# Kernel tuning notes

Measured on AMD Instinct MI355X. Metric: run time of the kernel, lower is better.

Reference implementation:

```python
import jax, jax.numpy as jnp
import numpy as np

B, S, HID = 2, 2048, 1024
H, D = 16, HID // 16  # heads, head_dim
ROPE_BASE = 10000.0


def setup_inputs() -> dict:
    key = jax.random.key(0)
    k1, k2, k3, k4 = jax.random.split(key, 4)
    scale = 1.0 / np.sqrt(HID)
    return {
        "hidden_states": jax.random.normal(k1, (B, S, HID), dtype=jnp.float32),
        "attention_mask": jnp.zeros((B, 1, 1, S), dtype=jnp.float32),
        "Wq": jax.random.normal(k2, (HID, HID), dtype=jnp.float32) * scale,
        "Wk": jax.random.normal(k3, (HID, HID), dtype=jnp.float32) * scale,
        "Wv": jax.random.normal(k4, (HID, HID), dtype=jnp.float32) * scale,
    }


def _rope_cos_sin(seq_len, dim, dtype):
    inv_freq = 1.0 / (ROPE_BASE ** (jnp.arange(0, dim, 2, dtype=jnp.float32) / dim))
    freqs = jnp.arange(seq_len, dtype=jnp.float32)[:, None] * inv_freq[None, :]  # (S, D/2)
    emb = jnp.concatenate([freqs, freqs], axis=-1)  # (S, D)
    return jnp.cos(emb).astype(dtype), jnp.sin(emb).astype(dtype)


def _rotate_half(x):
    x1, x2 = jnp.split(x, 2, axis=-1)
    return jnp.concatenate([-x2, x1], axis=-1)


def reference(hidden_states, attention_mask, Wq, Wk, Wv):
    b, s, _ = hidden_states.shape
    # QKV projections (no bias), split into heads: (b, H, s, D)
    def proj(W):
        return jnp.einsum('bse,de->bsd', hidden_states, W).reshape(b, s, H, D).transpose(0, 2, 1, 3)
    q, k, v = proj(Wq), proj(Wk), proj(Wv)
    # Rotary embedding on q, k over sequence positions
    cos, sin = _rope_cos_sin(s, D, hidden_states.dtype)  # (s, D)
    cos = cos[None, None]  # (1,1,s,D)
    sin = sin[None, None]
    q = q * cos + _rotate_half(q) * sin
    k = k * cos + _rotate_half(k) * sin
    # Scaled dot-product attention with additive mask
    scores = jnp.einsum('bhqd,bhkd->bhqk', q, k) / jnp.sqrt(jnp.asarray(D, hidden_states.dtype))
    scores = scores + attention_mask
    probs = jax.nn.softmax(scores, axis=-1)  # dropout p=0 (eval) -> identity
    ctx = jnp.einsum('bhqk,bhkd->bhqd', probs, v)
    return ctx.transpose(0, 2, 1, 3).reshape(b, s, H * D)
```

## Files before the change

### kernel.cpp

```cpp
#include <hip/hip_runtime.h>
#include <stdint.h>

typedef unsigned short u16;
typedef short bf16x8 __attribute__((ext_vector_type(8)));
typedef float f32x4 __attribute__((ext_vector_type(4)));

#define S_ 2048
#define HID_ 1024
#define H_ 16
#define D_ 64

#define LOG2E 1.4426950408889634f
#define SCALE_LOG2 0.18033688011112042f
#define MAXC_LOG2 11.541560327111707f

__device__ __forceinline__ u16 f2bf(float f) {
  uint32_t x = __builtin_bit_cast(uint32_t, f);
  uint32_t r = (x + 0x7fffu + ((x >> 16) & 1u)) >> 16;
  return (u16)r;
}
__device__ __forceinline__ uint32_t packbf2(float a, float b) {
  return (uint32_t)f2bf(a) | ((uint32_t)f2bf(b) << 16);
}
__device__ __forceinline__ uint32_t permpack(float a, float b) {
  return __builtin_amdgcn_perm(__builtin_bit_cast(uint32_t, b),
                               __builtin_bit_cast(uint32_t, a), 0x07060302u);
}

__device__ __forceinline__ void gl2lds16(const void* g, void* l) {
  __builtin_amdgcn_global_load_lds(
      (const __attribute__((address_space(1))) unsigned int*)g,
      (__attribute__((address_space(3))) unsigned int*)l, 16, 0, 0);
}

#define NX_ (1 << 20)
#define NW_ (1 << 18)
#define NROPE_ 65536
__global__ void prep_kernel(const float* __restrict__ X, const float* __restrict__ Wq,
                            const float* __restrict__ Wk, const float* __restrict__ Wv,
                            const float* __restrict__ mask, u16* __restrict__ Xb,
                            u16* __restrict__ Wqb, u16* __restrict__ Wkb,
                            u16* __restrict__ Wvb, float* __restrict__ cos_t,
                            float* __restrict__ sin_t, float* __restrict__ mask2) {
  int i = blockIdx.x * 256 + threadIdx.x;
  if (i < NX_ + 3 * NW_) {
    const float* src;
    u16* dst;
    int off;
    if (i < NX_) {
      src = X; dst = Xb; off = i;
    } else if (i < NX_ + NW_) {
      src = Wq; dst = Wqb; off = i - NX_;
    } else if (i < NX_ + 2 * NW_) {
      src = Wk; dst = Wkb; off = i - NX_ - NW_;
    } else {
      src = Wv; dst = Wvb; off = i - NX_ - 2 * NW_;
    }
    float4 v = ((const float4*)src)[off];
    uint2 packed;
    packed.x = packbf2(v.x, v.y);
    packed.y = packbf2(v.z, v.w);
    ((uint2*)dst)[off] = packed;
  } else if (i < NX_ + 3 * NW_ + NROPE_) {
    int t = i - (NX_ + 3 * NW_);
    int s = t >> 5, j = t & 31;
    float invf = powf(10000.0f, -(float)j * (1.0f / 32.0f));
    float ang = (float)s * invf;
    cos_t[t] = cosf(ang);
    sin_t[t] = sinf(ang);
  } else {
    int t = i - (NX_ + 3 * NW_ + NROPE_);
    mask2[t] = fmaf(mask[t], LOG2E, -MAXC_LOG2);
  }
}

__global__ __launch_bounds__(256) void qkv_gemm_kernel(
    const u16* __restrict__ X, const u16* __restrict__ Wq, const u16* __restrict__ Wk,
    const u16* __restrict__ Wv, const float* __restrict__ cos_t,
    const float* __restrict__ sin_t, u16* __restrict__ Q, u16* __restrict__ K,
    u16* __restrict__ Vt) {
  __shared__ char smem[65536];
  int tid = threadIdx.x;
  int lane = tid & 63, wave = tid >> 6;
  int wm = wave >> 1, wn = wave & 1;
  int quad = lane >> 4, l16 = lane & 15;
  int which = blockIdx.x >> 3;
  int nbase = (blockIdx.x & 7) * 128;
  int mbase = blockIdx.y * 128;
  const u16* W = (which == 0) ? Wq : (which == 1) ? Wk : Wv;

#pragma unroll
  for (int it = 0; it < 4; ++it) {
    int i = it * 256 + tid;
    int r = i >> 3, gs = i & 7, gsrc = gs ^ (r & 7);
    gl2lds16(X + (size_t)(mbase + r) * HID_ + gsrc * 8, smem + i * 16);
    gl2lds16(W + (size_t)(nbase + r) * HID_ + gsrc * 8, smem + 32768 + i * 16);
  }

  f32x4 acc[4][4] = {};

  for (int kk = 0; kk < 16; ++kk) {
    char* As = smem + (kk & 1) * 16384;
    char* Bs = smem + 32768 + (kk & 1) * 16384;
    __syncthreads();

    if (kk < 15) {
      int k0n = (kk + 1) * 64;
      char* An = smem + ((kk + 1) & 1) * 16384;
      char* Bn = smem + 32768 + ((kk + 1) & 1) * 16384;
#pragma unroll
      for (int it = 0; it < 4; ++it) {
        int i = it * 256 + tid;
        int r = i >> 3, gs = i & 7, gsrc = gs ^ (r & 7);
        gl2lds16(X + (size_t)(mbase + r) * HID_ + k0n + gsrc * 8, An + i * 16);
        gl2lds16(W + (size_t)(nbase + r) * HID_ + k0n + gsrc * 8, Bn + i * 16);
      }
    }

#pragma unroll
    for (int kh = 0; kh < 2; ++kh) {
      bf16x8 afrag[4], bfrag[4];
#pragma unroll
      for (int i4 = 0; i4 < 4; ++i4) {
        int r = wm * 64 + i4 * 16 + l16;
        int L = r * 8 + ((kh * 4 + quad) ^ (r & 7));
        afrag[i4] = *(const bf16x8*)(As + L * 16);
      }
#pragma unroll
      for (int j4 = 0; j4 < 4; ++j4) {
        int r = wn * 64 + j4 * 16 + l16;
        int L = r * 8 + ((kh * 4 + quad) ^ (r & 7));
        bfrag[j4] = *(const bf16x8*)(Bs + L * 16);
      }
      if (which == 2) {
#pragma unroll
        for (int i4 = 0; i4 < 4; ++i4)
#pragma unroll
          for (int j4 = 0; j4 < 4; ++j4)
            acc[i4][j4] = __builtin_amdgcn_mfma_f32_16x16x32_bf16(afrag[i4], bfrag[j4],
                                                                  acc[i4][j4], 0, 0, 0);
      } else {
#pragma unroll
        for (int i4 = 0; i4 < 4; ++i4)
#pragma unroll
          for (int j4 = 0; j4 < 4; ++j4)
            acc[i4][j4] = __builtin_amdgcn_mfma_f32_16x16x32_bf16(bfrag[j4], afrag[i4],
                                                                  acc[i4][j4], 0, 0, 0);
      }
    }
  }

  if (which == 2) {
#pragma unroll
    for (int i4 = 0; i4 < 4; ++i4)
#pragma unroll
      for (int j4 = 0; j4 < 4; ++j4) {
        int m = mbase + wm * 64 + i4 * 16 + quad * 4;
        int n = nbase + wn * 64 + j4 * 16 + l16;
        int b = m >> 11, s0 = m & 2047;
        int h = n >> 6, d = n & 63;
        uint2 pk;
        pk.x = packbf2(acc[i4][j4][0], acc[i4][j4][1]);
        pk.y = packbf2(acc[i4][j4][2], acc[i4][j4][3]);
        *(uint2*)(Vt + (((size_t)(b * H_ + h)) * D_ + d) * S_ + s0) = pk;
      }
  } else {
    u16* dst = (which == 0) ? Q : K;
#pragma unroll
    for (int i4 = 0; i4 < 4; ++i4)
#pragma unroll
      for (int j4 = 0; j4 < 2; ++j4) {
        int m = mbase + wm * 64 + i4 * 16 + l16;
        int n1 = nbase + wn * 64 + j4 * 16 + quad * 4;
        int b = m >> 11, s = m & 2047;
        int h = n1 >> 6, d1 = n1 & 63;
        float4 c4 = *(const float4*)(cos_t + s * 32 + d1);
        float4 s4 = *(const float4*)(sin_t + s * 32 + d1);
        float y1[4], y2[4];
#pragma unroll
        for (int r = 0; r < 4; ++r) {
          float cr = ((const float*)&c4)[r], sr = ((const float*)&s4)[r];
          float x1 = acc[i4][j4][r], x2 = acc[i4][j4 + 2][r];
          y1[r] = x1 * cr - x2 * sr;
          y2[r] = x2 * cr + x1 * sr;
        }
        size_t base = ((size_t)(b * H_ + h) * S_ + s) * D_;
        uint2 p1, p2;
        p1.x = packbf2(y1[0], y1[1]);
        p1.y = packbf2(y1[2], y1[3]);
        p2.x = packbf2(y2[0], y2[1]);
        p2.y = packbf2(y2[2], y2[3]);
        *(uint2*)(dst + base + d1) = p1;
        *(uint2*)(dst + base + d1 + 32) = p2;
      }
  }
}

__device__ __forceinline__ void pv_step(const bf16x8 (*pp)[2], const char* Vp, int quad,
                                        int l16, const bf16x8& ones, f32x4 (*o)[4],
                                        f32x4* lacc) {
  lacc[0] = __builtin_amdgcn_mfma_f32_16x16x32_bf16(pp[0][0], ones, lacc[0], 0, 0, 0);
  lacc[0] = __builtin_amdgcn_mfma_f32_16x16x32_bf16(pp[0][1], ones, lacc[0], 0, 0, 0);
  lacc[1] = __builtin_amdgcn_mfma_f32_16x16x32_bf16(pp[1][0], ones, lacc[1], 0, 0, 0);
  lacc[1] = __builtin_amdgcn_mfma_f32_16x16x32_bf16(pp[1][1], ones, lacc[1], 0, 0, 0);
#pragma unroll
  for (int jd = 0; jd < 4; ++jd) {
    int r = jd * 16 + l16;
#pragma unroll
    for (int kh = 0; kh < 2; ++kh) {
      int L = r * 8 + ((kh * 4 + quad) ^ (r & 7));
      bf16x8 vf = *(const bf16x8*)(Vp + L * 16);
      o[0][jd] = __builtin_amdgcn_mfma_f32_16x16x32_bf16(pp[0][kh], vf, o[0][jd], 0, 0, 0);
      o[1][jd] = __builtin_amdgcn_mfma_f32_16x16x32_bf16(pp[1][kh], vf, o[1][jd], 0, 0, 0);
    }
  }
}

__device__ __forceinline__ void qk_step(const char* Ks, const bf16x8 (*qfrag)[2], int quad,
                                        int l16, f32x4 (*s)[4]) {
#pragma unroll
  for (int jt = 0; jt < 4; ++jt) {
    int r = jt * 16 + l16;
#pragma unroll
    for (int kh = 0; kh < 2; ++kh) {
      int L = r * 8 + ((kh * 4 + quad) ^ (r & 7));
      bf16x8 kf = *(const bf16x8*)(Ks + L * 16);
      s[0][jt] = __builtin_amdgcn_mfma_f32_16x16x32_bf16(kf, qfrag[0][kh], s[0][jt], 0, 0, 0);
      s[1][jt] = __builtin_amdgcn_mfma_f32_16x16x32_bf16(kf, qfrag[1][kh], s[1][jt], 0, 0, 0);
    }
  }
}

__device__ __forceinline__ void softmax_pack(const f32x4 (*s)[4], const float4* mv,
                                             bf16x8 (*pp)[2]) {
#pragma unroll
  for (int qb = 0; qb < 2; ++qb) {
    uint32_t a[4][2];
#pragma unroll
    for (int jt = 0; jt < 4; ++jt) {
      float pf[4];
#pragma unroll
      for (int r = 0; r < 4; ++r) {
        float mvr = ((const float*)&mv[jt])[r];
        pf[r] = __builtin_amdgcn_exp2f(fmaf(s[qb][jt][r], SCALE_LOG2, mvr));
      }
      a[jt][0] = permpack(pf[0], pf[1]);
      a[jt][1] = permpack(pf[2], pf[3]);
    }
#pragma unroll
    for (int kh = 0; kh < 2; ++kh) {
      uint32_t tt[4];
#pragma unroll
      for (int i = 0; i < 2; ++i) {
        auto r1 = __builtin_amdgcn_permlane32_swap(a[2 * kh][i], a[2 * kh + 1][i],
                                                   false, false);
        auto r2 = __builtin_amdgcn_permlane16_swap(r1[0], r1[1], false, false);
        tt[i] = r2[0];
        tt[2 + i] = r2[1];
      }
      union { uint32_t u[4]; bf16x8 v; } cv;
      cv.u[0] = tt[0]; cv.u[1] = tt[1]; cv.u[2] = tt[2]; cv.u[3] = tt[3];
      pp[qb][kh] = cv.v;
    }
  }
}

__device__ __forceinline__ void stage_kv(const u16* Kbase, const u16* Vbase, char* Kn,
                                         int nb, int tid) {
#pragma unroll
  for (int half = 0; half < 2; ++half) {
    int i = half * 256 + tid;
    int r = i >> 3, gs = i & 7, gsrc = gs ^ (r & 7);
    gl2lds16(Kbase + (size_t)(nb + r) * D_ + gsrc * 8, Kn + i * 16);
    gl2lds16(Vbase + (size_t)r * S_ + nb + gsrc * 8, Kn + 8192 + i * 16);
  }
}

__global__ __launch_bounds__(256, 2) void flash_kernel(
    const u16* __restrict__ Q, const u16* __restrict__ K, const u16* __restrict__ Vt,
    const float* __restrict__ mask2, float* __restrict__ out) {
  __shared__ char smem[49152];
  int tid = threadIdx.x, wave = tid >> 6;
  int lane = tid & 63;
  int quad = lane >> 4, l16 = lane & 15;
  int bh = blockIdx.y, b = bh >> 4, h = bh & 15;
  int qbase = blockIdx.x * 128;
  int qw = qbase + wave * 32;
  const float* m2row = mask2 + b * S_;
  const u16* Kbase = K + (size_t)bh * S_ * D_;
  const u16* Vbase = Vt + (size_t)bh * D_ * S_;

  bf16x8 qfrag[2][2];
#pragma unroll
  for (int qb = 0; qb < 2; ++qb) {
    const u16* qp = Q + ((size_t)bh * S_ + qw + qb * 16 + l16) * D_ + quad * 8;
    qfrag[qb][0] = *(const bf16x8*)qp;
    qfrag[qb][1] = *(const bf16x8*)(qp + 32);
  }
  bf16x8 ones;
#pragma unroll
  for (int j = 0; j < 8; ++j) ones[j] = (short)0x3f80;

  f32x4 o[2][4] = {};
  f32x4 lacc[2] = {};
  bf16x8 pp[2][2];

  stage_kv(Kbase, Vbase, smem, 0, tid);
  float4 mv[4];
#pragma unroll
  for (int jt = 0; jt < 4; ++jt) mv[jt] = *(const float4*)(m2row + jt * 16 + quad * 4);

  {
    __syncthreads();
    stage_kv(Kbase, Vbase, smem + 16384, 64, tid);
    f32x4 s[2][4] = {};
    __builtin_amdgcn_s_setprio(1);
    qk_step(smem, qfrag, quad, l16, s);
    __builtin_amdgcn_s_setprio(0);
    softmax_pack(s, mv, pp);
#pragma unroll
    for (int jt = 0; jt < 4; ++jt)
      mv[jt] = *(const float4*)(m2row + 64 + jt * 16 + quad * 4);
  }

  for (int kt = 1; kt <= 30; ++kt) {
    char* Ks = smem + (kt % 3) * 16384;
    __syncthreads();
    stage_kv(Kbase, Vbase, smem + ((kt + 1) % 3) * 16384, (kt + 1) * 64, tid);

    __builtin_amdgcn_s_setprio(1);
    const char* Vp = smem + ((kt - 1) % 3) * 16384 + 8192;
    pv_step(pp, Vp, quad, l16, ones, o, lacc);

    f32x4 s[2][4] = {};
    qk_step(Ks, qfrag, quad, l16, s);
    __builtin_amdgcn_s_setprio(0);

    softmax_pack(s, mv, pp);
#pragma unroll
    for (int jt = 0; jt < 4; ++jt)
      mv[jt] = *(const float4*)(m2row + (kt + 1) * 64 + jt * 16 + quad * 4);
  }

  {
    __syncthreads();
    __builtin_amdgcn_s_setprio(1);
    pv_step(pp, smem + 0 * 16384 + 8192, quad, l16, ones, o, lacc);
    f32x4 s[2][4] = {};
    qk_step(smem + 16384, qfrag, quad, l16, s);
    __builtin_amdgcn_s_setprio(0);
    softmax_pack(s, mv, pp);
  }

  pv_step(pp, smem + 16384 + 8192, quad, l16, ones, o, lacc);

  float inv[2][4];
#pragma unroll
  for (int qb = 0; qb < 2; ++qb)
#pragma unroll
    for (int r = 0; r < 4; ++r) inv[qb][r] = 1.0f / lacc[qb][r];
#pragma unroll
  for (int qb = 0; qb < 2; ++qb)
#pragma unroll
    for (int jd = 0; jd < 4; ++jd) {
#pragma unroll
      for (int r = 0; r < 4; ++r) {
        int d = jd * 16 + l16;
        int q = qw + qb * 16 + quad * 4 + r;
        out[(((size_t)b * S_ + q) * H_ + h) * D_ + d] = o[qb][jd][r] * inv[qb][r];
      }
    }
}

extern "C" void kernel_launch(void* const* d_in, const int* in_sizes, int n_in,
                              void* d_out, int out_size, void* d_ws, size_t ws_size,
                              hipStream_t stream) {
  const float* hid = (const float*)d_in[0];
  const float* mask = (const float*)d_in[1];
  const float* Wq = (const float*)d_in[2];
  const float* Wk = (const float*)d_in[3];
  const float* Wv = (const float*)d_in[4];
  float* out = (float*)d_out;
  char* ws = (char*)d_ws;

  u16* Xbf = (u16*)ws;
  u16* Wqb = (u16*)(ws + (8u << 20));
  u16* Wkb = (u16*)(ws + (10u << 20));
  u16* Wvb = (u16*)(ws + (12u << 20));
  u16* Qb = (u16*)(ws + (14u << 20));
  u16* Kb = (u16*)(ws + (22u << 20));
  u16* Vtb = (u16*)(ws + (30u << 20));
  float* cos_t = (float*)(ws + (38u << 20));
  float* sin_t = (float*)(ws + (38u << 20) + (256u << 10));
  float* mask2 = (float*)(ws + (38u << 20) + (512u << 10));

  prep_kernel<<<7440, 256, 0, stream>>>(hid, Wq, Wk, Wv, mask, Xbf, Wqb, Wkb, Wvb,
                                        cos_t, sin_t, mask2);
  qkv_gemm_kernel<<<dim3(24, 32), 256, 0, stream>>>(Xbf, Wqb, Wkb, Wvb, cos_t, sin_t,
                                                    Qb, Kb, Vtb);
  flash_kernel<<<dim3(16, 32), 256, 0, stream>>>(Qb, Kb, Vtb, mask2, out);
}
```

Baseline: 168.3 us.

## Split attention over two key halves and combine partial results

The flash kernel now splits the key sequence into two halves along a third grid dimension, doubling the block count from 512 to 1024. Each half writes unnormalized partial outputs and row sums, and a new combine kernel adds them and normalizes. LDS buffers are reorganized (K double-buffered, V triple-buffered, 40KB) and launch bounds are raised to 4 blocks per CU to improve occupancy. Correctness depends on the softmax using a fixed max constant rather than a running max, so the two partials can simply be summed. The split costs an extra kernel launch plus extra global writes and reads of a partial output buffer.

```diff
diff --git a/kernel.cpp b/kernel.cpp
--- a/kernel.cpp
+++ b/kernel.cpp
@@ -265,25 +265,28 @@
   }
 }
 
-__device__ __forceinline__ void stage_kv(const u16* Kbase, const u16* Vbase, char* Kn,
-                                         int nb, int tid) {
-#pragma unroll
-  for (int half = 0; half < 2; ++half) {
-    int i = half * 256 + tid;
+__device__ __forceinline__ void stage_kv(const u16* Kbase, const u16* Vbase, char* Kd,
+                                         char* Vd, int nb, int tid) {
+#pragma unroll
+  for (int hh = 0; hh < 2; ++hh) {
+    int i = hh * 256 + tid;
     int r = i >> 3, gs = i & 7, gsrc = gs ^ (r & 7);
-    gl2lds16(Kbase + (size_t)(nb + r) * D_ + gsrc * 8, Kn + i * 16);
-    gl2lds16(Vbase + (size_t)r * S_ + nb + gsrc * 8, Kn + 8192 + i * 16);
-  }
-}
-
-__global__ __launch_bounds__(256, 2) void flash_kernel(
+    gl2lds16(Kbase + (size_t)(nb + r) * D_ + gsrc * 8, Kd + i * 16);
+    gl2lds16(Vbase + (size_t)r * S_ + nb + gsrc * 8, Vd + i * 16);
+  }
+}
+
+__global__ __launch_bounds__(256, 4) void flash_kernel(
     const u16* __restrict__ Q, const u16* __restrict__ K, const u16* __restrict__ Vt,
-    const float* __restrict__ mask2, float* __restrict__ out) {
-  __shared__ char smem[49152];
+    const float* __restrict__ mask2, float* __restrict__ out0, float* __restrict__ po1,
+    float* __restrict__ pl) {
+  __shared__ char smem[40960];
   int tid = threadIdx.x, wave = tid >> 6;
   int lane = tid & 63;
   int quad = lane >> 4, l16 = lane & 15;
   int bh = blockIdx.y, b = bh >> 4, h = bh & 15;
+  int half = blockIdx.z;
+  int khbase = half << 10;
   int qbase = blockIdx.x * 128;
   int qw = qbase + wave * 32;
   const float* m2row = mask2 + b * S_;
@@ -305,14 +308,15 @@
   f32x4 lacc[2] = {};
   bf16x8 pp[2][2];
 
-  stage_kv(Kbase, Vbase, smem, 0, tid);
+  stage_kv(Kbase, Vbase, smem, smem + 16384, khbase, tid);
   float4 mv[4];
 #pragma unroll
-  for (int jt = 0; jt < 4; ++jt) mv[jt] = *(const float4*)(m2row + jt * 16 + quad * 4);
+  for (int jt = 0; jt < 4; ++jt)
+    mv[jt] = *(const float4*)(m2row + khbase + jt * 16 + quad * 4);
 
   {
     __syncthreads();
-    stage_kv(Kbase, Vbase, smem + 16384, 64, tid);
+    stage_kv(Kbase, Vbase, smem + 8192, smem + 16384 + 8192, khbase + 64, tid);
     f32x4 s[2][4] = {};
     __builtin_amdgcn_s_setprio(1);
     qk_step(smem, qfrag, quad, l16, s);
@@ -320,45 +324,40 @@
     softmax_pack(s, mv, pp);
 #pragma unroll
     for (int jt = 0; jt < 4; ++jt)
-      mv[jt] = *(const float4*)(m2row + 64 + jt * 16 + quad * 4);
-  }
-
-  for (int kt = 1; kt <= 30; ++kt) {
-    char* Ks = smem + (kt % 3) * 16384;
+      mv[jt] = *(const float4*)(m2row + khbase + 64 + jt * 16 + quad * 4);
+  }
+
+  for (int t = 1; t <= 14; ++t) {
     __syncthreads();
-    stage_kv(Kbase, Vbase, smem + ((kt + 1) % 3) * 16384, (kt + 1) * 64, tid);
+    stage_kv(Kbase, Vbase, smem + ((t + 1) & 1) * 8192,
+             smem + 16384 + ((t + 1) % 3) * 8192, khbase + (t + 1) * 64, tid);
 
     __builtin_amdgcn_s_setprio(1);
-    const char* Vp = smem + ((kt - 1) % 3) * 16384 + 8192;
-    pv_step(pp, Vp, quad, l16, ones, o, lacc);
+    pv_step(pp, smem + 16384 + ((t - 1) % 3) * 8192, quad, l16, ones, o, lacc);
 
     f32x4 s[2][4] = {};
-    qk_step(Ks, qfrag, quad, l16, s);
+    qk_step(smem + (t & 1) * 8192, qfrag, quad, l16, s);
     __builtin_amdgcn_s_setprio(0);
 
     softmax_pack(s, mv, pp);
 #pragma unroll
     for (int jt = 0; jt < 4; ++jt)
-      mv[jt] = *(const float4*)(m2row + (kt + 1) * 64 + jt * 16 + quad * 4);
+      mv[jt] = *(const float4*)(m2row + khbase + (t + 1) * 64 + jt * 16 + quad * 4);
   }
 
   {
     __syncthreads();
     __builtin_amdgcn_s_setprio(1);
-    pv_step(pp, smem + 0 * 16384 + 8192, quad, l16, ones, o, lacc);
+    pv_step(pp, smem + 16384 + 2 * 8192, quad, l16, ones, o, lacc);
     f32x4 s[2][4] = {};
-    qk_step(smem + 16384, qfrag, quad, l16, s);
+    qk_step(smem + 8192, qfrag, quad, l16, s);
     __builtin_amdgcn_s_setprio(0);
     softmax_pack(s, mv, pp);
   }
 
-  pv_step(pp, smem + 16384 + 8192, quad, l16, ones, o, lacc);
-
-  float inv[2][4];
-#pragma unroll
-  for (int qb = 0; qb < 2; ++qb)
-#pragma unroll
-    for (int r = 0; r < 4; ++r) inv[qb][r] = 1.0f / lacc[qb][r];
+  pv_step(pp, smem + 16384, quad, l16, ones, o, lacc);
+
+  float* dst = (half == 0) ? out0 : po1;
 #pragma unroll
   for (int qb = 0; qb < 2; ++qb)
 #pragma unroll
@@ -367,9 +366,37 @@
       for (int r = 0; r < 4; ++r) {
         int d = jd * 16 + l16;
         int q = qw + qb * 16 + quad * 4 + r;
-        out[(((size_t)b * S_ + q) * H_ + h) * D_ + d] = o[qb][jd][r] * inv[qb][r];
-      }
-    }
+        dst[(((size_t)b * S_ + q) * H_ + h) * D_ + d] = o[qb][jd][r];
+      }
+    }
+  if (l16 == 0) {
+#pragma unroll
+    for (int qb = 0; qb < 2; ++qb)
+#pragma unroll
+      for (int r = 0; r < 4; ++r) {
+        int q = qw + qb * 16 + quad * 4 + r;
+        pl[(half << 16) + bh * S_ + q] = lacc[qb][r];
+      }
+  }
+}
+
+__global__ __launch_bounds__(256) void combine_kernel(float* __restrict__ out,
+                                                      const float* __restrict__ po1,
+                                                      const float* __restrict__ pl) {
+  int i = blockIdx.x * 256 + threadIdx.x;
+  int h = (i >> 4) & 15;
+  int q = (i >> 8) & 2047;
+  int b = i >> 19;
+  int bhq = (b * 16 + h) * 2048 + q;
+  float4 a = ((const float4*)out)[i];
+  float4 c = ((const float4*)po1)[i];
+  float inv = 1.0f / (pl[bhq] + pl[65536 + bhq]);
+  float4 r;
+  r.x = (a.x + c.x) * inv;
+  r.y = (a.y + c.y) * inv;
+  r.z = (a.z + c.z) * inv;
+  r.w = (a.w + c.w) * inv;
+  ((float4*)out)[i] = r;
 }
 
 extern "C" void kernel_launch(void* const* d_in, const int* in_sizes, int n_in,
@@ -393,10 +420,13 @@
   float* cos_t = (float*)(ws + (38u << 20));
   float* sin_t = (float*)(ws + (38u << 20) + (256u << 10));
   float* mask2 = (float*)(ws + (38u << 20) + (512u << 10));
+  float* po1 = (float*)(ws + (40u << 20));
+  float* pl = (float*)(ws + (56u << 20));
 
   prep_kernel<<<7440, 256, 0, stream>>>(hid, Wq, Wk, Wv, mask, Xbf, Wqb, Wkb, Wvb,
                                         cos_t, sin_t, mask2);
   qkv_gemm_kernel<<<dim3(24, 32), 256, 0, stream>>>(Xbf, Wqb, Wkb, Wvb, cos_t, sin_t,
                                                     Qb, Kb, Vtb);
-  flash_kernel<<<dim3(16, 32), 256, 0, stream>>>(Qb, Kb, Vtb, mask2, out);
-}
+  flash_kernel<<<dim3(16, 32, 2), 256, 0, stream>>>(Qb, Kb, Vtb, mask2, out, po1, pl);
+  combine_kernel<<<4096, 256, 0, stream>>>(out, po1, pl);
+}
```

Measured after the change: 180.8 us. 1.07x slower.

## Fuse Q/K/V projections into one block sharing the staged X tile

Applied to the files above, without the earlier changes.

Each QKV GEMM block now computes the same 128x128 output tile for all three weight matrices. It stages X once per k-step alongside the Wq, Wk and Wv tiles, using 512 threads and a 128KB double-buffered LDS. This removes the threefold redundant loading of X tiles across separate blocks and cuts the grid from 768 to 256 blocks. The cost is lower occupancy, since LDS use allows only one block per CU. It also produces a single wave of blocks with less latency hiding, plus more accumulator registers per wave.

```diff
diff --git a/kernel.cpp b/kernel.cpp
--- a/kernel.cpp
+++ b/kernel.cpp
@@ -74,125 +74,133 @@
   }
 }
 
-__global__ __launch_bounds__(256) void qkv_gemm_kernel(
+__global__ __launch_bounds__(512, 2) void qkv_gemm_kernel(
     const u16* __restrict__ X, const u16* __restrict__ Wq, const u16* __restrict__ Wk,
     const u16* __restrict__ Wv, const float* __restrict__ cos_t,
     const float* __restrict__ sin_t, u16* __restrict__ Q, u16* __restrict__ K,
     u16* __restrict__ Vt) {
-  __shared__ char smem[65536];
+  __shared__ char smem[131072];
   int tid = threadIdx.x;
   int lane = tid & 63, wave = tid >> 6;
-  int wm = wave >> 1, wn = wave & 1;
+  int wm = wave >> 2, wn = wave & 3;
   int quad = lane >> 4, l16 = lane & 15;
-  int which = blockIdx.x >> 3;
-  int nbase = (blockIdx.x & 7) * 128;
+  int nbase = blockIdx.x * 128;
   int mbase = blockIdx.y * 128;
-  const u16* W = (which == 0) ? Wq : (which == 1) ? Wk : Wv;
-
-#pragma unroll
-  for (int it = 0; it < 4; ++it) {
-    int i = it * 256 + tid;
-    int r = i >> 3, gs = i & 7, gsrc = gs ^ (r & 7);
-    gl2lds16(X + (size_t)(mbase + r) * HID_ + gsrc * 8, smem + i * 16);
-    gl2lds16(W + (size_t)(nbase + r) * HID_ + gsrc * 8, smem + 32768 + i * 16);
-  }
-
-  f32x4 acc[4][4] = {};
+
+#define STAGE_ALL(k0, buf)                                                        \
+  {                                                                               \
+    _Pragma("unroll") for (int it = 0; it < 8; ++it) {                            \
+      int j = (it & 1) * 512 + tid;                                               \
+      int r = j >> 3, gs = j & 7, gsrc = gs ^ (r & 7);                            \
+      const u16* src; int rb;                                                     \
+      if ((it >> 1) == 0)      { src = X;  rb = mbase + r; }                      \
+      else if ((it >> 1) == 1) { src = Wq; rb = nbase + r; }                      \
+      else if ((it >> 1) == 2) { src = Wk; rb = nbase + r; }                      \
+      else                     { src = Wv; rb = nbase + r; }                      \
+      gl2lds16(src + (size_t)rb * HID_ + (k0) + gsrc * 8,                         \
+               (buf) + (it >> 1) * 16384 + j * 16);                               \
+    }                                                                             \
+  }
+
+  STAGE_ALL(0, smem)
+
+  f32x4 acc[3][4][2] = {};
 
   for (int kk = 0; kk < 16; ++kk) {
-    char* As = smem + (kk & 1) * 16384;
-    char* Bs = smem + 32768 + (kk & 1) * 16384;
+    const char* buf = smem + (kk & 1) * 65536;
     __syncthreads();
 
-    if (kk < 15) {
-      int k0n = (kk + 1) * 64;
-      char* An = smem + ((kk + 1) & 1) * 16384;
-      char* Bn = smem + 32768 + ((kk + 1) & 1) * 16384;
-#pragma unroll
-      for (int it = 0; it < 4; ++it) {
-        int i = it * 256 + tid;
-        int r = i >> 3, gs = i & 7, gsrc = gs ^ (r & 7);
-        gl2lds16(X + (size_t)(mbase + r) * HID_ + k0n + gsrc * 8, An + i * 16);
-        gl2lds16(W + (size_t)(nbase + r) * HID_ + k0n + gsrc * 8, Bn + i * 16);
-      }
-    }
+    if (kk < 15)
+      STAGE_ALL((kk + 1) * 64, smem + ((kk + 1) & 1) * 65536)
 
 #pragma unroll
     for (int kh = 0; kh < 2; ++kh) {
-      bf16x8 afrag[4], bfrag[4];
+      bf16x8 afrag[4];
 #pragma unroll
       for (int i4 = 0; i4 < 4; ++i4) {
         int r = wm * 64 + i4 * 16 + l16;
         int L = r * 8 + ((kh * 4 + quad) ^ (r & 7));
-        afrag[i4] = *(const bf16x8*)(As + L * 16);
-      }
-#pragma unroll
-      for (int j4 = 0; j4 < 4; ++j4) {
-        int r = wn * 64 + j4 * 16 + l16;
-        int L = r * 8 + ((kh * 4 + quad) ^ (r & 7));
-        bfrag[j4] = *(const bf16x8*)(Bs + L * 16);
-      }
-      if (which == 2) {
-#pragma unroll
-        for (int i4 = 0; i4 < 4; ++i4)
-#pragma unroll
-          for (int j4 = 0; j4 < 4; ++j4)
-            acc[i4][j4] = __builtin_amdgcn_mfma_f32_16x16x32_bf16(afrag[i4], bfrag[j4],
-                                                                  acc[i4][j4], 0, 0, 0);
-      } else {
-#pragma unroll
-        for (int i4 = 0; i4 < 4; ++i4)
-#pragma unroll
-          for (int j4 = 0; j4 < 4; ++j4)
-            acc[i4][j4] = __builtin_amdgcn_mfma_f32_16x16x32_bf16(bfrag[j4], afrag[i4],
-                                                                  acc[i4][j4], 0, 0, 0);
-      }
-    }
-  }
-
-  if (which == 2) {
-#pragma unroll
-    for (int i4 = 0; i4 < 4; ++i4)
-#pragma unroll
-      for (int j4 = 0; j4 < 4; ++j4) {
-        int m = mbase + wm * 64 + i4 * 16 + quad * 4;
-        int n = nbase + wn * 64 + j4 * 16 + l16;
-        int b = m >> 11, s0 = m & 2047;
-        int h = n >> 6, d = n & 63;
-        uint2 pk;
-        pk.x = packbf2(acc[i4][j4][0], acc[i4][j4][1]);
-        pk.y = packbf2(acc[i4][j4][2], acc[i4][j4][3]);
-        *(uint2*)(Vt + (((size_t)(b * H_ + h)) * D_ + d) * S_ + s0) = pk;
-      }
-  } else {
-    u16* dst = (which == 0) ? Q : K;
-#pragma unroll
-    for (int i4 = 0; i4 < 4; ++i4)
-#pragma unroll
-      for (int j4 = 0; j4 < 2; ++j4) {
-        int m = mbase + wm * 64 + i4 * 16 + l16;
-        int n1 = nbase + wn * 64 + j4 * 16 + quad * 4;
-        int b = m >> 11, s = m & 2047;
-        int h = n1 >> 6, d1 = n1 & 63;
-        float4 c4 = *(const float4*)(cos_t + s * 32 + d1);
-        float4 s4 = *(const float4*)(sin_t + s * 32 + d1);
-        float y1[4], y2[4];
-#pragma unroll
-        for (int r = 0; r < 4; ++r) {
-          float cr = ((const float*)&c4)[r], sr = ((const float*)&s4)[r];
-          float x1 = acc[i4][j4][r], x2 = acc[i4][j4 + 2][r];
-          y1[r] = x1 * cr - x2 * sr;
-          y2[r] = x2 * cr + x1 * sr;
+        afrag[i4] = *(const bf16x8*)(buf + L * 16);
+      }
+#pragma unroll
+      for (int w = 0; w < 3; ++w) {
+        const char* Bs = buf + 16384 + w * 16384;
+        bf16x8 bfrag[2];
+#pragma unroll
+        for (int j2 = 0; j2 < 2; ++j2) {
+          int r = (wn >> 1) * 64 + (wn & 1) * 16 + j2 * 32 + l16;
+          int L = r * 8 + ((kh * 4 + quad) ^ (r & 7));
+          bfrag[j2] = *(const bf16x8*)(Bs + L * 16);
         }
-        size_t base = ((size_t)(b * H_ + h) * S_ + s) * D_;
-        uint2 p1, p2;
-        p1.x = packbf2(y1[0], y1[1]);
-        p1.y = packbf2(y1[2], y1[3]);
-        p2.x = packbf2(y2[0], y2[1]);
-        p2.y = packbf2(y2[2], y2[3]);
-        *(uint2*)(dst + base + d1) = p1;
-        *(uint2*)(dst + base + d1 + 32) = p2;
-      }
+        if (w == 2) {
+#pragma unroll
+          for (int i4 = 0; i4 < 4; ++i4)
+#pragma unroll
+            for (int j2 = 0; j2 < 2; ++j2)
+              acc[2][i4][j2] = __builtin_amdgcn_mfma_f32_16x16x32_bf16(
+                  afrag[i4], bfrag[j2], acc[2][i4][j2], 0, 0, 0);
+        } else if (w == 1) {
+#pragma unroll
+          for (int i4 = 0; i4 < 4; ++i4)
+#pragma unroll
+            for (int j2 = 0; j2 < 2; ++j2)
+              acc[1][i4][j2] = __builtin_amdgcn_mfma_f32_16x16x32_bf16(
+                  bfrag[j2], afrag[i4], acc[1][i4][j2], 0, 0, 0);
+        } else {
+#pragma unroll
+          for (int i4 = 0; i4 < 4; ++i4)
+#pragma unroll
+            for (int j2 = 0; j2 < 2; ++j2)
+              acc[0][i4][j2] = __builtin_amdgcn_mfma_f32_16x16x32_bf16(
+                  bfrag[j2], afrag[i4], acc[0][i4][j2], 0, 0, 0);
+        }
+      }
+    }
+  }
+#undef STAGE_ALL
+
+#pragma unroll
+  for (int i4 = 0; i4 < 4; ++i4)
+#pragma unroll
+    for (int j2 = 0; j2 < 2; ++j2) {
+      int m = mbase + wm * 64 + i4 * 16 + quad * 4;
+      int n = nbase + (wn >> 1) * 64 + (wn & 1) * 16 + j2 * 32 + l16;
+      int b = m >> 11, s0 = m & 2047;
+      int h = n >> 6, d = n & 63;
+      uint2 pk;
+      pk.x = packbf2(acc[2][i4][j2][0], acc[2][i4][j2][1]);
+      pk.y = packbf2(acc[2][i4][j2][2], acc[2][i4][j2][3]);
+      *(uint2*)(Vt + (((size_t)(b * H_ + h)) * D_ + d) * S_ + s0) = pk;
+    }
+
+#pragma unroll
+  for (int w = 0; w < 2; ++w) {
+    u16* dst = (w == 0) ? Q : K;
+#pragma unroll
+    for (int i4 = 0; i4 < 4; ++i4) {
+      int m = mbase + wm * 64 + i4 * 16 + l16;
+      int n1 = nbase + (wn >> 1) * 64 + (wn & 1) * 16 + quad * 4;
+      int b = m >> 11, s = m & 2047;
+      int h = n1 >> 6, d1 = n1 & 63;
+      float4 c4 = *(const float4*)(cos_t + s * 32 + d1);
+      float4 s4 = *(const float4*)(sin_t + s * 32 + d1);
+      float y1[4], y2[4];
+#pragma unroll
+      for (int r = 0; r < 4; ++r) {
+        float cr = ((const float*)&c4)[r], sr = ((const float*)&s4)[r];
+        float x1 = acc[w][i4][0][r], x2 = acc[w][i4][1][r];
+        y1[r] = x1 * cr - x2 * sr;
+        y2[r] = x2 * cr + x1 * sr;
+      }
+      size_t base = ((size_t)(b * H_ + h) * S_ + s) * D_;
+      uint2 p1, p2;
+      p1.x = packbf2(y1[0], y1[1]);
+      p1.y = packbf2(y1[2], y1[3]);
+      p2.x = packbf2(y2[0], y2[1]);
+      p2.y = packbf2(y2[2], y2[3]);
+      *(uint2*)(dst + base + d1) = p1;
+      *(uint2*)(dst + base + d1 + 32) = p2;
+    }
   }
 }
 
@@ -396,7 +404,7 @@
 
   prep_kernel<<<7440, 256, 0, stream>>>(hid, Wq, Wk, Wv, mask, Xbf, Wqb, Wkb, Wvb,
                                         cos_t, sin_t, mask2);
-  qkv_gemm_kernel<<<dim3(24, 32), 256, 0, stream>>>(Xbf, Wqb, Wkb, Wvb, cos_t, sin_t,
-                                                    Qb, Kb, Vtb);
+  qkv_gemm_kernel<<<dim3(8, 32), 512, 0, stream>>>(Xbf, Wqb, Wkb, Wvb, cos_t, sin_t,
+                                                   Qb, Kb, Vtb);
   flash_kernel<<<dim3(16, 32), 256, 0, stream>>>(Qb, Kb, Vtb, mask2, out);
 }
```

New measurement: 160.2 us. 4.8% less time.
